# Kernel optimization log

Hardware: AMD Instinct MI355X
Metric: run time of the kernel (lower is better)

Reference implementation:

```python
import jax, jax.numpy as jnp
import numpy as np

VOCAB = 32000
DEMBED = 512


def embed_position(dembed):
    # Faithful to the torch code: ep[1::2] = ep[0::2]; ep = 1/10000**(ep/dembed);
    # pos = arange(dembed) * ep; odd -> cos, even -> sin.
    i = jnp.arange(dembed, dtype=jnp.float32)
    ep_idx = jnp.floor(i / 2.0) * 2.0           # even index duplicated to the following odd slot
    ep = 1.0 / jnp.power(10000.0, ep_idx / dembed)
    pos = i * ep
    is_odd = (jnp.arange(dembed) % 2) == 1
    return jnp.where(is_odd, jnp.cos(pos), jnp.sin(pos))  # [dembed]


def setup_inputs() -> dict:
    key = jax.random.key(0)
    k1, k2 = jax.random.split(key)
    x = jax.random.randint(k1, (64, 1024), 0, VOCAB, dtype=jnp.int64)
    table = jax.random.normal(k2, (VOCAB, DEMBED), dtype=jnp.float32)
    return {"x": x, "table": table}


def reference(x, table):
    # one-hot matmul == direct gather; fuse with positional add
    pos = embed_position(table.shape[1])         # [dembed]
    return table[x] + pos                        # [B, S, dembed]
```

## Files before the change

kernel.cpp:

```cpp
#include <hip/hip_runtime.h>
#include <hip/hip_bf16.h>
#include <math.h>

#define DEMBED 512
#define NTOK (64 * 1024)

__global__ void pos_kernel(float* __restrict__ pos) {
    int i = threadIdx.x;
    if (i < DEMBED) {
        float ep_idx = (float)((i / 2) * 2);
        float ep = 1.0f / powf(10000.0f, ep_idx / (float)DEMBED);
        float p = (float)i * ep;
        pos[i] = (i & 1) ? cosf(p) : sinf(p);
    }
}

__global__ void __launch_bounds__(256)
embed_kernel(const int* __restrict__ x,
             const float* __restrict__ table,
             const float* __restrict__ pos,
             float* __restrict__ out,
             int n4)
{
    const float4* __restrict__ t4 = (const float4*)table;
    const float4* __restrict__ p4 = (const float4*)pos;
    float4* __restrict__ o4 = (float4*)out;

    int stride = gridDim.x * blockDim.x;
    for (int gid = blockIdx.x * blockDim.x + threadIdx.x; gid < n4; gid += stride) {
        int tok = gid >> 7;
        int d4  = gid & 127;
        int row = x[tok];
        float4 t = t4[(size_t)row * 128 + d4];
        float4 p = p4[d4];
        float4 r;
        r.x = t.x + p.x; r.y = t.y + p.y; r.z = t.z + p.z; r.w = t.w + p.w;
        o4[gid] = r;
    }
}

extern "C" void kernel_launch(void* const* d_in, const int* in_sizes, int n_in,
                              void* d_out, int out_size, void* d_ws, size_t ws_size,
                              hipStream_t stream) {
    const int*   x     = (const int*)d_in[0];
    const float* table = (const float*)d_in[1];
    float*       out   = (float*)d_out;
    float*       pos   = (float*)d_ws;

    pos_kernel<<<1, DEMBED, 0, stream>>>(pos);

    int n4 = NTOK * (DEMBED / 4);
    int blocks = 2048;
    embed_kernel<<<blocks, 256, 0, stream>>>(x, table, pos, out, n4);
}
```

Before: 48.84 us.

## Fuse positional encoding into embed kernel, unroll fixed loop, nontemporal stores

Removes the separate pos_kernel launch and computes each thread's four positional values in registers. This works because the stride is a multiple of 128, so a thread's d4 slot never changes across iterations. The grid-stride loop becomes a fully unrolled compile-time count, and output writes use nontemporal stores so the large write-once output does not pollute the cache. The cost is some transcendental math per thread, and the positional values now come from expf with a log constant instead of powf, which may differ slightly in the last bits.

```diff
diff --git a/kernel.cpp b/kernel.cpp
--- a/kernel.cpp
+++ b/kernel.cpp
@@ -3,39 +3,45 @@
 #include <math.h>
 
 #define DEMBED 512
-#define NTOK (64 * 1024)
+#define NTOK   (64 * 1024)
+#define TPB    256
+#define BLOCKS 2048
+#define STRIDE (BLOCKS * TPB)
+#define N4     (NTOK * (DEMBED / 4))
+#define ITERS  (N4 / STRIDE)
 
-__global__ void pos_kernel(float* __restrict__ pos) {
-    int i = threadIdx.x;
-    if (i < DEMBED) {
-        float ep_idx = (float)((i / 2) * 2);
-        float ep = 1.0f / powf(10000.0f, ep_idx / (float)DEMBED);
-        float p = (float)i * ep;
-        pos[i] = (i & 1) ? cosf(p) : sinf(p);
-    }
-}
+typedef float f4 __attribute__((ext_vector_type(4)));
 
-__global__ void __launch_bounds__(256)
+__global__ void __launch_bounds__(TPB)
 embed_kernel(const int* __restrict__ x,
              const float* __restrict__ table,
-             const float* __restrict__ pos,
-             float* __restrict__ out,
-             int n4)
+             float* __restrict__ out)
 {
-    const float4* __restrict__ t4 = (const float4*)table;
-    const float4* __restrict__ p4 = (const float4*)pos;
-    float4* __restrict__ o4 = (float4*)out;
+    const int tid = blockIdx.x * TPB + threadIdx.x;
+    const int d4  = tid & 127;
 
-    int stride = gridDim.x * blockDim.x;
-    for (int gid = blockIdx.x * blockDim.x + threadIdx.x; gid < n4; gid += stride) {
+    f4 p;
+    const float kLog = logf(10000.0f) / (float)DEMBED;
+#pragma unroll
+    for (int j = 0; j < 4; ++j) {
+        int   i      = d4 * 4 + j;
+        float ep_idx = (float)(i & ~1);
+        float ep     = expf(-ep_idx * kLog);
+        float ang    = (float)i * ep;
+        p[j] = (i & 1) ? cosf(ang) : sinf(ang);
+    }
+
+    const f4* __restrict__ t4 = (const f4*)table;
+    f4*       __restrict__ o4 = (f4*)out;
+
+#pragma unroll
+    for (int it = 0; it < ITERS; ++it) {
+        int gid = tid + it * STRIDE;
         int tok = gid >> 7;
-        int d4  = gid & 127;
         int row = x[tok];
-        float4 t = t4[(size_t)row * 128 + d4];
-        float4 p = p4[d4];
-        float4 r;
-        r.x = t.x + p.x; r.y = t.y + p.y; r.z = t.z + p.z; r.w = t.w + p.w;
-        o4[gid] = r;
+        f4  t   = t4[(size_t)row * 128 + d4];
+        f4  r   = t + p;
+        __builtin_nontemporal_store(r, &o4[gid]);
     }
 }
 
@@ -45,11 +51,6 @@
     const int*   x     = (const int*)d_in[0];
     const float* table = (const float*)d_in[1];
     float*       out   = (float*)d_out;
-    float*       pos   = (float*)d_ws;
 
-    pos_kernel<<<1, DEMBED, 0, stream>>>(pos);
-
-    int n4 = NTOK * (DEMBED / 4);
-    int blocks = 2048;
-    embed_kernel<<<blocks, 256, 0, stream>>>(x, table, pos, out, n4);
+    embed_kernel<<<BLOCKS, TPB, 0, stream>>>(x, table, out);
 }
```

Result: no change. 48.39 us (-0.9%).
